# Kernel optimization log

Hardware: AMD Instinct MI355X
Metric: run time of the kernel (lower is better)

Reference implementation:

```python
import jax, jax.numpy as jnp
import numpy as np

L, B, D = 4096, 4, 1024

def setup_inputs() -> dict:
    key = jax.random.key(0)
    k1, k2, k3, k4 = jax.random.split(key, 4)
    return {
        "x": jax.random.normal(k1, (L, B, D), dtype=jnp.float32),
        "lmlg": jax.random.normal(k2, (D,), dtype=jnp.float32),
        "theta": jax.random.normal(k3, (D,), dtype=jnp.float32),
        "last_conv_init": jax.random.normal(k4, (D,), dtype=jnp.float32),
    }

def reference(x, lmlg, theta, last_conv_init):
    seq_len, batch, dim = x.shape
    # per-channel decay*rotation: c = gamma * e^{i*theta}, gamma = exp(-exp(lmlg))
    gamma = jnp.exp(-jnp.exp(lmlg))                       # [D]
    c = gamma * jnp.exp(1j * theta)                       # [D] complex64
    # causal filter c^n for n = 0..L-1
    n = jnp.arange(seq_len)[:, None]                      # [L,1]
    filt = c[None, :] ** n                                # [L,D] complex64
    # linear (causal) convolution via zero-padded FFT of length 2L
    filt_fft = jnp.fft.fft(filt, n=2 * seq_len, axis=0)   # [2L,D]
    x_fft = jnp.fft.fft(x, n=2 * seq_len, axis=0)         # [2L,B,D]
    conv_filter_x = jnp.fft.ifft(filt_fft[:, None, :] * x_fft, axis=0)[:seq_len]  # [L,B,D]
    # carry-in state (fresh state = last_conv_init expanded; detached in torch)
    last_conv = jax.lax.stop_gradient(
        jnp.broadcast_to(last_conv_init.astype(conv_filter_x.dtype), (batch, dim))
    )                                                     # [B,D]
    conv_with_past = conv_filter_x + last_conv[None, :, :] * filt[:, None, :] * c[None, None, :]
    return conv_with_past.real * x
```

## Files before the change

kernel.cpp:

```cpp
#include <hip/hip_runtime.h>


#define L_  4096
#define B_  4
#define D_  1024
#define BD_ (B_ * D_)

__global__ __launch_bounds__(256) void sc_phase1(
    const float* __restrict__ x,
    const float* __restrict__ lmlg,
    const float* __restrict__ theta,
    float2* __restrict__ ws, int ch) {
  const int t  = threadIdx.x;
  const int k  = blockIdx.x / B_;
  const int b  = blockIdx.x % B_;
  const int d0 = t * 4;

  float4 lg = *(const float4*)(lmlg + d0);
  float4 th = *(const float4*)(theta + d0);
  float cr[4], ci[4], sr[4] = {0.f,0.f,0.f,0.f}, si[4] = {0.f,0.f,0.f,0.f};
  {
    float g0 = expf(-expf(lg.x)), g1 = expf(-expf(lg.y));
    float g2 = expf(-expf(lg.z)), g3 = expf(-expf(lg.w));
    cr[0] = g0 * cosf(th.x); ci[0] = g0 * sinf(th.x);
    cr[1] = g1 * cosf(th.y); ci[1] = g1 * sinf(th.y);
    cr[2] = g2 * cosf(th.z); ci[2] = g2 * sinf(th.z);
    cr[3] = g3 * cosf(th.w); ci[3] = g3 * sinf(th.w);
  }

  const float* xp = x + (size_t)k * ch * BD_ + (size_t)b * D_ + d0;
#pragma unroll 4
  for (int j = 0; j < ch; ++j) {
    float4 xv = *(const float4*)(xp + (size_t)j * BD_);
    float xa[4] = {xv.x, xv.y, xv.z, xv.w};
#pragma unroll
    for (int q = 0; q < 4; ++q) {
      float nr = fmaf(cr[q], sr[q], fmaf(-ci[q], si[q], xa[q]));
      float ni = fmaf(cr[q], si[q], ci[q] * sr[q]);
      sr[q] = nr; si[q] = ni;
    }
  }

  float2* wp = ws + (size_t)k * BD_ + (size_t)b * D_ + d0;
  wp[0] = make_float2(sr[0], si[0]);
  wp[1] = make_float2(sr[1], si[1]);
  wp[2] = make_float2(sr[2], si[2]);
  wp[3] = make_float2(sr[3], si[3]);
}

__global__ __launch_bounds__(256) void sc_phase2(
    const float* __restrict__ lmlg,
    const float* __restrict__ theta,
    const float* __restrict__ init,
    float2* __restrict__ ws, int nc, float chf) {
  const int idx = blockIdx.x * 256 + threadIdx.x;
  const int d   = idx & (D_ - 1);
  float e  = expf(lmlg[d]);
  float th = theta[d];
  float gC = expf(-e * chf);
  float aC = th * chf;
  float Cr = gC * cosf(aC), Ci = gC * sinf(aC);
  float hr = init[d], hi = 0.f;
  for (int k = 0; k < nc; ++k) {
    float2 s = ws[(size_t)k * BD_ + idx];
    ws[(size_t)k * BD_ + idx] = make_float2(hr, hi);
    float nr = fmaf(Cr, hr, fmaf(-Ci, hi, s.x));
    float ni = fmaf(Cr, hi, fmaf(Ci, hr, s.y));
    hr = nr; hi = ni;
  }
}

__global__ __launch_bounds__(256) void sc_phase3(
    const float* __restrict__ x,
    const float* __restrict__ lmlg,
    const float* __restrict__ theta,
    const float2* __restrict__ ws,
    float* __restrict__ out, int ch) {
  const int t  = threadIdx.x;
  const int k  = blockIdx.x / B_;
  const int b  = blockIdx.x % B_;
  const int d0 = t * 4;

  float4 lg = *(const float4*)(lmlg + d0);
  float4 th = *(const float4*)(theta + d0);
  float cr[4], ci[4];
  {
    float g0 = expf(-expf(lg.x)), g1 = expf(-expf(lg.y));
    float g2 = expf(-expf(lg.z)), g3 = expf(-expf(lg.w));
    cr[0] = g0 * cosf(th.x); ci[0] = g0 * sinf(th.x);
    cr[1] = g1 * cosf(th.y); ci[1] = g1 * sinf(th.y);
    cr[2] = g2 * cosf(th.z); ci[2] = g2 * sinf(th.z);
    cr[3] = g3 * cosf(th.w); ci[3] = g3 * sinf(th.w);
  }

  const float2* wp = ws + (size_t)k * BD_ + (size_t)b * D_ + d0;
  float hr[4], hi[4];
#pragma unroll
  for (int q = 0; q < 4; ++q) { float2 h = wp[q]; hr[q] = h.x; hi[q] = h.y; }

  const size_t off = (size_t)k * ch * BD_ + (size_t)b * D_ + d0;
  const float* xp = x + off;
  float*       op = out + off;
#pragma unroll 4
  for (int j = 0; j < ch; ++j) {
    float4 xv = *(const float4*)(xp + (size_t)j * BD_);
    float xa[4] = {xv.x, xv.y, xv.z, xv.w};
    float4 res;
    float* ra = &res.x;
#pragma unroll
    for (int q = 0; q < 4; ++q) {
      float nr = fmaf(cr[q], hr[q], fmaf(-ci[q], hi[q], xa[q]));
      float ni = fmaf(cr[q], hi[q], ci[q] * hr[q]);
      hr[q] = nr; hi[q] = ni;
      ra[q] = nr * xa[q];
    }
    *(float4*)(op + (size_t)j * BD_) = res;
  }
}

__global__ __launch_bounds__(256) void sc_full(
    const float* __restrict__ x,
    const float* __restrict__ lmlg,
    const float* __restrict__ theta,
    const float* __restrict__ init,
    float* __restrict__ out) {
  const int idx = blockIdx.x * 256 + threadIdx.x;
  const int d   = idx & (D_ - 1);
  float g  = expf(-expf(lmlg[d]));
  float cr = g * cosf(theta[d]), ci = g * sinf(theta[d]);
  float hr = init[d], hi = 0.f;
  const float* xp = x + idx;
  float*       op = out + idx;
  for (int n = 0; n < L_; ++n) {
    float xv = xp[(size_t)n * BD_];
    float nr = fmaf(cr, hr, fmaf(-ci, hi, xv));
    float ni = fmaf(cr, hi, ci * hr);
    hr = nr; hi = ni;
    op[(size_t)n * BD_] = nr * xv;
  }
}

extern "C" void kernel_launch(void* const* d_in, const int* in_sizes, int n_in,
                              void* d_out, int out_size, void* d_ws, size_t ws_size,
                              hipStream_t stream) {
  const float* x     = (const float*)d_in[0];
  const float* lmlg  = (const float*)d_in[1];
  const float* theta = (const float*)d_in[2];
  const float* init  = (const float*)d_in[3];
  float*  out = (float*)d_out;
  float2* ws  = (float2*)d_ws;

  const size_t row_bytes = (size_t)BD_ * sizeof(float2);
  int nc = 128;
  while (nc > 1 && (size_t)nc * row_bytes > ws_size) nc >>= 1;

  if (nc >= 2 && (size_t)nc * row_bytes <= ws_size) {
    const int ch = L_ / nc;
    sc_phase1<<<nc * B_, 256, 0, stream>>>(x, lmlg, theta, ws, ch);
    sc_phase2<<<BD_ / 256, 256, 0, stream>>>(lmlg, theta, init, ws, nc, (float)ch);
    sc_phase3<<<nc * B_, 256, 0, stream>>>(x, lmlg, theta, ws, out, ch);
  } else {
    sc_full<<<BD_ / 256, 256, 0, stream>>>(x, lmlg, theta, init, out);
  }
}
```

Baseline: 159.8 us.

## Fold the chunk-carry scan into the output kernel, dropping a launch

Removes the separate carry-propagation kernel. Each output block now rebuilds its incoming state by serially combining all earlier chunk sums using c^ch. This saves one launch and the serial 16-block pass over the workspace. In exchange, later chunks redo up to nc-1 combine steps and redundant workspace reads, so the work is quadratic in nc and late blocks finish behind early ones.

```diff
diff --git a/kernel.cpp b/kernel.cpp
--- a/kernel.cpp
+++ b/kernel.cpp
@@ -6,7 +6,7 @@
 #define D_  1024
 #define BD_ (B_ * D_)
 
-__global__ __launch_bounds__(256) void sc_phase1(
+__global__ __launch_bounds__(256) void sc_sum(
     const float* __restrict__ x,
     const float* __restrict__ lmlg,
     const float* __restrict__ theta,
@@ -41,39 +41,18 @@
     }
   }
 
-  float2* wp = ws + (size_t)k * BD_ + (size_t)b * D_ + d0;
+  float2* wp = ws + (size_t)(k * B_ + b) * D_ + d0;
   wp[0] = make_float2(sr[0], si[0]);
   wp[1] = make_float2(sr[1], si[1]);
   wp[2] = make_float2(sr[2], si[2]);
   wp[3] = make_float2(sr[3], si[3]);
 }
 
-__global__ __launch_bounds__(256) void sc_phase2(
+__global__ __launch_bounds__(256) void sc_out(
+    const float* __restrict__ x,
     const float* __restrict__ lmlg,
     const float* __restrict__ theta,
     const float* __restrict__ init,
-    float2* __restrict__ ws, int nc, float chf) {
-  const int idx = blockIdx.x * 256 + threadIdx.x;
-  const int d   = idx & (D_ - 1);
-  float e  = expf(lmlg[d]);
-  float th = theta[d];
-  float gC = expf(-e * chf);
-  float aC = th * chf;
-  float Cr = gC * cosf(aC), Ci = gC * sinf(aC);
-  float hr = init[d], hi = 0.f;
-  for (int k = 0; k < nc; ++k) {
-    float2 s = ws[(size_t)k * BD_ + idx];
-    ws[(size_t)k * BD_ + idx] = make_float2(hr, hi);
-    float nr = fmaf(Cr, hr, fmaf(-Ci, hi, s.x));
-    float ni = fmaf(Cr, hi, fmaf(Ci, hr, s.y));
-    hr = nr; hi = ni;
-  }
-}
-
-__global__ __launch_bounds__(256) void sc_phase3(
-    const float* __restrict__ x,
-    const float* __restrict__ lmlg,
-    const float* __restrict__ theta,
     const float2* __restrict__ ws,
     float* __restrict__ out, int ch) {
   const int t  = threadIdx.x;
@@ -93,10 +72,33 @@
     cr[3] = g3 * cosf(th.w); ci[3] = g3 * sinf(th.w);
   }
 
-  const float2* wp = ws + (size_t)k * BD_ + (size_t)b * D_ + d0;
-  float hr[4], hi[4];
+  const float chf = (float)ch;
+  float Cr[4], Ci[4];
+  {
+    float e0 = expf(lg.x), e1 = expf(lg.y), e2 = expf(lg.z), e3 = expf(lg.w);
+    float g0 = expf(-e0 * chf), g1 = expf(-e1 * chf);
+    float g2 = expf(-e2 * chf), g3 = expf(-e3 * chf);
+    Cr[0] = g0 * cosf(th.x * chf); Ci[0] = g0 * sinf(th.x * chf);
+    Cr[1] = g1 * cosf(th.y * chf); Ci[1] = g1 * sinf(th.y * chf);
+    Cr[2] = g2 * cosf(th.z * chf); Ci[2] = g2 * sinf(th.z * chf);
+    Cr[3] = g3 * cosf(th.w * chf); Ci[3] = g3 * sinf(th.w * chf);
+  }
+
+  float4 iv = *(const float4*)(init + d0);
+  float hr[4] = {iv.x, iv.y, iv.z, iv.w};
+  float hi[4] = {0.f, 0.f, 0.f, 0.f};
+  for (int kk = 0; kk < k; ++kk) {
+    const float2* sp = ws + (size_t)(kk * B_ + b) * D_ + d0;
+    float2 s0 = sp[0], s1 = sp[1], s2 = sp[2], s3 = sp[3];
+    float sxr[4] = {s0.x, s1.x, s2.x, s3.x};
+    float sxi[4] = {s0.y, s1.y, s2.y, s3.y};
 #pragma unroll
-  for (int q = 0; q < 4; ++q) { float2 h = wp[q]; hr[q] = h.x; hi[q] = h.y; }
+    for (int q = 0; q < 4; ++q) {
+      float nr = fmaf(Cr[q], hr[q], fmaf(-Ci[q], hi[q], sxr[q]));
+      float ni = fmaf(Cr[q], hi[q], fmaf(Ci[q], hr[q], sxi[q]));
+      hr[q] = nr; hi[q] = ni;
+    }
+  }
 
   const size_t off = (size_t)k * ch * BD_ + (size_t)b * D_ + d0;
   const float* xp = x + off;
@@ -105,8 +107,7 @@
   for (int j = 0; j < ch; ++j) {
     float4 xv = *(const float4*)(xp + (size_t)j * BD_);
     float xa[4] = {xv.x, xv.y, xv.z, xv.w};
-    float4 res;
-    float* ra = &res.x;
+    float4 res; float* ra = &res.x;
 #pragma unroll
     for (int q = 0; q < 4; ++q) {
       float nr = fmaf(cr[q], hr[q], fmaf(-ci[q], hi[q], xa[q]));
@@ -119,14 +120,12 @@
 }
 
 __global__ __launch_bounds__(256) void sc_full(
-    const float* __restrict__ x,
-    const float* __restrict__ lmlg,
-    const float* __restrict__ theta,
-    const float* __restrict__ init,
+    const float* __restrict__ x, const float* __restrict__ lmlg,
+    const float* __restrict__ theta, const float* __restrict__ init,
     float* __restrict__ out) {
   const int idx = blockIdx.x * 256 + threadIdx.x;
   const int d   = idx & (D_ - 1);
-  float g  = expf(-expf(lmlg[d]));
+  float g = expf(-expf(lmlg[d]));
   float cr = g * cosf(theta[d]), ci = g * sinf(theta[d]);
   float hr = init[d], hi = 0.f;
   const float* xp = x + idx;
@@ -156,9 +155,8 @@
 
   if (nc >= 2 && (size_t)nc * row_bytes <= ws_size) {
     const int ch = L_ / nc;
-    sc_phase1<<<nc * B_, 256, 0, stream>>>(x, lmlg, theta, ws, ch);
-    sc_phase2<<<BD_ / 256, 256, 0, stream>>>(lmlg, theta, init, ws, nc, (float)ch);
-    sc_phase3<<<nc * B_, 256, 0, stream>>>(x, lmlg, theta, ws, out, ch);
+    sc_sum<<<nc * B_, 256, 0, stream>>>(x, lmlg, theta, ws, ch);
+    sc_out<<<nc * B_, 256, 0, stream>>>(x, lmlg, theta, init, ws, out, ch);
   } else {
     sc_full<<<BD_ / 256, 256, 0, stream>>>(x, lmlg, theta, init, out);
   }
```

Result: faster. 148.9 us (-6.8%).

## Split chunk scan into sub-groups with LDS combine and parallel carry kernel

Applied to the files above, without the earlier changes.

Each chunk of 32 timesteps is now split into four 8-step sub-groups per block, with partial sums combined through shared memory using c^8 powers. This raises the block count and shortens each thread's serial dependency chain. The carry kernel now runs one thread per (chunk, column) and recomputes the prefix over earlier chunks instead of running one serial loop per column. That adds redundant O(NC^2) reads of the small sum buffer and needs twice the workspace, falling back to the single-pass kernel if workspace is too small.

```diff
diff --git a/kernel.cpp b/kernel.cpp
--- a/kernel.cpp
+++ b/kernel.cpp
@@ -5,128 +5,219 @@
 #define B_  4
 #define D_  1024
 #define BD_ (B_ * D_)
-
-__global__ __launch_bounds__(256) void sc_phase1(
+#define NC  128
+#define CH  32
+#define NG  4
+#define GS  8
+#define SLICES 4
+#define LDSP 9
+
+__device__ __forceinline__ void make_c(const float4& lg, const float4& th,
+                                       float* cr, float* ci) {
+  float g0 = expf(-expf(lg.x)), g1 = expf(-expf(lg.y));
+  float g2 = expf(-expf(lg.z)), g3 = expf(-expf(lg.w));
+  cr[0] = g0 * cosf(th.x); ci[0] = g0 * sinf(th.x);
+  cr[1] = g1 * cosf(th.y); ci[1] = g1 * sinf(th.y);
+  cr[2] = g2 * cosf(th.z); ci[2] = g2 * sinf(th.z);
+  cr[3] = g3 * cosf(th.w); ci[3] = g3 * sinf(th.w);
+}
+__device__ __forceinline__ void make_c8(const float4& lg, const float4& th,
+                                        float* Cr, float* Ci) {
+  const float gs = (float)GS;
+  float e0 = expf(lg.x), e1 = expf(lg.y), e2 = expf(lg.z), e3 = expf(lg.w);
+  float g0 = expf(-e0 * gs), g1 = expf(-e1 * gs);
+  float g2 = expf(-e2 * gs), g3 = expf(-e3 * gs);
+  Cr[0] = g0 * cosf(th.x * gs); Ci[0] = g0 * sinf(th.x * gs);
+  Cr[1] = g1 * cosf(th.y * gs); Ci[1] = g1 * sinf(th.y * gs);
+  Cr[2] = g2 * cosf(th.z * gs); Ci[2] = g2 * sinf(th.z * gs);
+  Cr[3] = g3 * cosf(th.w * gs); Ci[3] = g3 * sinf(th.w * gs);
+}
+
+__global__ __launch_bounds__(256) void k_sum(
     const float* __restrict__ x,
     const float* __restrict__ lmlg,
     const float* __restrict__ theta,
-    float2* __restrict__ ws, int ch) {
+    float2* __restrict__ ws_sum) {
   const int t  = threadIdx.x;
-  const int k  = blockIdx.x / B_;
-  const int b  = blockIdx.x % B_;
-  const int d0 = t * 4;
+  const int g  = t >> 6;
+  const int q  = t & 63;
+  const int bid = blockIdx.x;
+  const int k   = bid / (B_ * SLICES);
+  const int rem = bid % (B_ * SLICES);
+  const int b   = rem / SLICES;
+  const int sl  = rem % SLICES;
+  const int d0  = sl * 256 + q * 4;
 
   float4 lg = *(const float4*)(lmlg + d0);
   float4 th = *(const float4*)(theta + d0);
-  float cr[4], ci[4], sr[4] = {0.f,0.f,0.f,0.f}, si[4] = {0.f,0.f,0.f,0.f};
+  float cr[4], ci[4];
+  make_c(lg, th, cr, ci);
+
+  const size_t base = (size_t)(k * CH + g * GS) * BD_ + (size_t)b * D_ + d0;
+  float4 xv[GS];
+#pragma unroll
+  for (int j = 0; j < GS; ++j)
+    xv[j] = *(const float4*)(x + base + (size_t)j * BD_);
+
+  float sr[4] = {0.f,0.f,0.f,0.f}, si[4] = {0.f,0.f,0.f,0.f};
+#pragma unroll
+  for (int j = 0; j < GS; ++j) {
+    const float* xa = &xv[j].x;
+#pragma unroll
+    for (int c = 0; c < 4; ++c) {
+      float nr = fmaf(cr[c], sr[c], fmaf(-ci[c], si[c], xa[c]));
+      float ni = fmaf(cr[c], si[c], ci[c] * sr[c]);
+      sr[c] = nr; si[c] = ni;
+    }
+  }
+
+  __shared__ float lds[NG * 64 * LDSP];
   {
-    float g0 = expf(-expf(lg.x)), g1 = expf(-expf(lg.y));
-    float g2 = expf(-expf(lg.z)), g3 = expf(-expf(lg.w));
-    cr[0] = g0 * cosf(th.x); ci[0] = g0 * sinf(th.x);
-    cr[1] = g1 * cosf(th.y); ci[1] = g1 * sinf(th.y);
-    cr[2] = g2 * cosf(th.z); ci[2] = g2 * sinf(th.z);
-    cr[3] = g3 * cosf(th.w); ci[3] = g3 * sinf(th.w);
-  }
-
-  const float* xp = x + (size_t)k * ch * BD_ + (size_t)b * D_ + d0;
-#pragma unroll 4
-  for (int j = 0; j < ch; ++j) {
-    float4 xv = *(const float4*)(xp + (size_t)j * BD_);
-    float xa[4] = {xv.x, xv.y, xv.z, xv.w};
-#pragma unroll
-    for (int q = 0; q < 4; ++q) {
-      float nr = fmaf(cr[q], sr[q], fmaf(-ci[q], si[q], xa[q]));
-      float ni = fmaf(cr[q], si[q], ci[q] * sr[q]);
-      sr[q] = nr; si[q] = ni;
-    }
-  }
-
-  float2* wp = ws + (size_t)k * BD_ + (size_t)b * D_ + d0;
-  wp[0] = make_float2(sr[0], si[0]);
-  wp[1] = make_float2(sr[1], si[1]);
-  wp[2] = make_float2(sr[2], si[2]);
-  wp[3] = make_float2(sr[3], si[3]);
-}
-
-__global__ __launch_bounds__(256) void sc_phase2(
+    float* p = &lds[(g * 64 + q) * LDSP];
+#pragma unroll
+    for (int c = 0; c < 4; ++c) { p[2*c] = sr[c]; p[2*c+1] = si[c]; }
+  }
+  __syncthreads();
+
+  if (g == 0) {
+    float Cr[4], Ci[4];
+    make_c8(lg, th, Cr, Ci);
+    float ar[4], ai[4];
+#pragma unroll
+    for (int c = 0; c < 4; ++c) { ar[c] = sr[c]; ai[c] = si[c]; }
+    for (int gg = 1; gg < NG; ++gg) {
+      const float* p = &lds[(gg * 64 + q) * LDSP];
+#pragma unroll
+      for (int c = 0; c < 4; ++c) {
+        float pr = p[2*c], pi = p[2*c+1];
+        float nr = fmaf(Cr[c], ar[c], fmaf(-Ci[c], ai[c], pr));
+        float ni = fmaf(Cr[c], ai[c], fmaf(Ci[c], ar[c], pi));
+        ar[c] = nr; ai[c] = ni;
+      }
+    }
+    float2* sp = ws_sum + (size_t)k * BD_ + (size_t)b * D_ + d0;
+#pragma unroll
+    for (int c = 0; c < 4; ++c) sp[c] = make_float2(ar[c], ai[c]);
+  }
+}
+
+__global__ __launch_bounds__(256) void k_carry(
     const float* __restrict__ lmlg,
     const float* __restrict__ theta,
     const float* __restrict__ init,
-    float2* __restrict__ ws, int nc, float chf) {
+    const float2* __restrict__ ws_sum,
+    float2* __restrict__ ws_carry) {
   const int idx = blockIdx.x * 256 + threadIdx.x;
-  const int d   = idx & (D_ - 1);
+  const int k   = idx >> 12;
+  const int col = idx & (BD_ - 1);
+  const int d   = col & (D_ - 1);
   float e  = expf(lmlg[d]);
   float th = theta[d];
-  float gC = expf(-e * chf);
-  float aC = th * chf;
+  float gC = expf(-e * (float)CH);
+  float aC = th * (float)CH;
   float Cr = gC * cosf(aC), Ci = gC * sinf(aC);
   float hr = init[d], hi = 0.f;
-  for (int k = 0; k < nc; ++k) {
-    float2 s = ws[(size_t)k * BD_ + idx];
-    ws[(size_t)k * BD_ + idx] = make_float2(hr, hi);
+  const float2* sp = ws_sum + col;
+  for (int kk = 0; kk < k; ++kk) {
+    float2 s = sp[(size_t)kk * BD_];
     float nr = fmaf(Cr, hr, fmaf(-Ci, hi, s.x));
     float ni = fmaf(Cr, hi, fmaf(Ci, hr, s.y));
     hr = nr; hi = ni;
   }
-}
-
-__global__ __launch_bounds__(256) void sc_phase3(
+  ws_carry[(size_t)k * BD_ + col] = make_float2(hr, hi);
+}
+
+__global__ __launch_bounds__(256) void k_out(
     const float* __restrict__ x,
     const float* __restrict__ lmlg,
     const float* __restrict__ theta,
-    const float2* __restrict__ ws,
-    float* __restrict__ out, int ch) {
+    const float2* __restrict__ ws_carry,
+    float* __restrict__ out) {
   const int t  = threadIdx.x;
-  const int k  = blockIdx.x / B_;
-  const int b  = blockIdx.x % B_;
-  const int d0 = t * 4;
+  const int g  = t >> 6;
+  const int q  = t & 63;
+  const int bid = blockIdx.x;
+  const int k   = bid / (B_ * SLICES);
+  const int rem = bid % (B_ * SLICES);
+  const int b   = rem / SLICES;
+  const int sl  = rem % SLICES;
+  const int d0  = sl * 256 + q * 4;
 
   float4 lg = *(const float4*)(lmlg + d0);
   float4 th = *(const float4*)(theta + d0);
   float cr[4], ci[4];
+  make_c(lg, th, cr, ci);
+
+  const size_t base = (size_t)(k * CH + g * GS) * BD_ + (size_t)b * D_ + d0;
+  float4 xv[GS];
+#pragma unroll
+  for (int j = 0; j < GS; ++j)
+    xv[j] = *(const float4*)(x + base + (size_t)j * BD_);
+
+  float sr[4] = {0.f,0.f,0.f,0.f}, si[4] = {0.f,0.f,0.f,0.f};
+#pragma unroll
+  for (int j = 0; j < GS; ++j) {
+    const float* xa = &xv[j].x;
+#pragma unroll
+    for (int c = 0; c < 4; ++c) {
+      float nr = fmaf(cr[c], sr[c], fmaf(-ci[c], si[c], xa[c]));
+      float ni = fmaf(cr[c], si[c], ci[c] * sr[c]);
+      sr[c] = nr; si[c] = ni;
+    }
+  }
+
+  __shared__ float lds[NG * 64 * LDSP];
   {
-    float g0 = expf(-expf(lg.x)), g1 = expf(-expf(lg.y));
-    float g2 = expf(-expf(lg.z)), g3 = expf(-expf(lg.w));
-    cr[0] = g0 * cosf(th.x); ci[0] = g0 * sinf(th.x);
-    cr[1] = g1 * cosf(th.y); ci[1] = g1 * sinf(th.y);
-    cr[2] = g2 * cosf(th.z); ci[2] = g2 * sinf(th.z);
-    cr[3] = g3 * cosf(th.w); ci[3] = g3 * sinf(th.w);
-  }
-
-  const float2* wp = ws + (size_t)k * BD_ + (size_t)b * D_ + d0;
+    float* p = &lds[(g * 64 + q) * LDSP];
+#pragma unroll
+    for (int c = 0; c < 4; ++c) { p[2*c] = sr[c]; p[2*c+1] = si[c]; }
+  }
+
   float hr[4], hi[4];
-#pragma unroll
-  for (int q = 0; q < 4; ++q) { float2 h = wp[q]; hr[q] = h.x; hi[q] = h.y; }
-
-  const size_t off = (size_t)k * ch * BD_ + (size_t)b * D_ + d0;
-  const float* xp = x + off;
-  float*       op = out + off;
-#pragma unroll 4
-  for (int j = 0; j < ch; ++j) {
-    float4 xv = *(const float4*)(xp + (size_t)j * BD_);
-    float xa[4] = {xv.x, xv.y, xv.z, xv.w};
-    float4 res;
-    float* ra = &res.x;
-#pragma unroll
-    for (int q = 0; q < 4; ++q) {
-      float nr = fmaf(cr[q], hr[q], fmaf(-ci[q], hi[q], xa[q]));
-      float ni = fmaf(cr[q], hi[q], ci[q] * hr[q]);
-      hr[q] = nr; hi[q] = ni;
-      ra[q] = nr * xa[q];
-    }
-    *(float4*)(op + (size_t)j * BD_) = res;
+  {
+    const float2* cp = ws_carry + (size_t)k * BD_ + (size_t)b * D_ + d0;
+#pragma unroll
+    for (int c = 0; c < 4; ++c) { float2 h = cp[c]; hr[c] = h.x; hi[c] = h.y; }
+  }
+  __syncthreads();
+
+  if (g > 0) {
+    float Cr[4], Ci[4];
+    make_c8(lg, th, Cr, Ci);
+    for (int i = 0; i < g; ++i) {
+      const float* p = &lds[(i * 64 + q) * LDSP];
+#pragma unroll
+      for (int c = 0; c < 4; ++c) {
+        float pr = p[2*c], pi = p[2*c+1];
+        float nr = fmaf(Cr[c], hr[c], fmaf(-Ci[c], hi[c], pr));
+        float ni = fmaf(Cr[c], hi[c], fmaf(Ci[c], hr[c], pi));
+        hr[c] = nr; hi[c] = ni;
+      }
+    }
+  }
+
+#pragma unroll
+  for (int j = 0; j < GS; ++j) {
+    const float* xa = &xv[j].x;
+    float4 res; float* ra = &res.x;
+#pragma unroll
+    for (int c = 0; c < 4; ++c) {
+      float nr = fmaf(cr[c], hr[c], fmaf(-ci[c], hi[c], xa[c]));
+      float ni = fmaf(cr[c], hi[c], ci[c] * hr[c]);
+      hr[c] = nr; hi[c] = ni;
+      ra[c] = nr * xa[c];
+    }
+    *(float4*)(out + base + (size_t)j * BD_) = res;
   }
 }
 
 __global__ __launch_bounds__(256) void sc_full(
-    const float* __restrict__ x,
-    const float* __restrict__ lmlg,
-    const float* __restrict__ theta,
-    const float* __restrict__ init,
+    const float* __restrict__ x, const float* __restrict__ lmlg,
+    const float* __restrict__ theta, const float* __restrict__ init,
     float* __restrict__ out) {
   const int idx = blockIdx.x * 256 + threadIdx.x;
   const int d   = idx & (D_ - 1);
-  float g  = expf(-expf(lmlg[d]));
+  float g = expf(-expf(lmlg[d]));
   float cr = g * cosf(theta[d]), ci = g * sinf(theta[d]);
   float hr = init[d], hi = 0.f;
   const float* xp = x + idx;
@@ -148,17 +239,14 @@
   const float* theta = (const float*)d_in[2];
   const float* init  = (const float*)d_in[3];
   float*  out = (float*)d_out;
-  float2* ws  = (float2*)d_ws;
-
-  const size_t row_bytes = (size_t)BD_ * sizeof(float2);
-  int nc = 128;
-  while (nc > 1 && (size_t)nc * row_bytes > ws_size) nc >>= 1;
-
-  if (nc >= 2 && (size_t)nc * row_bytes <= ws_size) {
-    const int ch = L_ / nc;
-    sc_phase1<<<nc * B_, 256, 0, stream>>>(x, lmlg, theta, ws, ch);
-    sc_phase2<<<BD_ / 256, 256, 0, stream>>>(lmlg, theta, init, ws, nc, (float)ch);
-    sc_phase3<<<nc * B_, 256, 0, stream>>>(x, lmlg, theta, ws, out, ch);
+
+  const size_t need = (size_t)2 * NC * BD_ * sizeof(float2);
+  if (ws_size >= need) {
+    float2* ws_sum   = (float2*)d_ws;
+    float2* ws_carry = ws_sum + (size_t)NC * BD_;
+    k_sum  <<<NC * B_ * SLICES, 256, 0, stream>>>(x, lmlg, theta, ws_sum);
+    k_carry<<<NC * BD_ / 256,   256, 0, stream>>>(lmlg, theta, init, ws_sum, ws_carry);
+    k_out  <<<NC * B_ * SLICES, 256, 0, stream>>>(x, lmlg, theta, ws_carry, out);
   } else {
     sc_full<<<BD_ / 256, 256, 0, stream>>>(x, lmlg, theta, init, out);
   }
```

After: 164.9 us. 3.2% more time.
